# Kernel tuning notes

Measured on AMD Instinct MI355X. Metric: run time of the kernel, lower is better.

## Reference

```python
import jax, jax.numpy as jnp
import numpy as np

K = 3
PAD = 1
STRIDE = 1
DIL = 1


def _bilinear_gather(feat, y, x):
    # feat: [B,C,H,W]; y,x: [B,KK,H,W] sampling coords -> [B,C,KK,H,W]
    B, C, H, W = feat.shape
    feat_flat = feat.reshape(B, C, H * W)
    y0 = jnp.floor(y)
    x0 = jnp.floor(x)
    out = jnp.zeros((B, C) + y.shape[1:], feat.dtype)
    for yi in (y0, y0 + 1.0):
        for xi in (x0, x0 + 1.0):
            wgt = (1.0 - jnp.abs(y - yi)) * (1.0 - jnp.abs(x - xi))
            valid = (yi >= 0) & (yi <= H - 1) & (xi >= 0) & (xi <= W - 1)
            yc = jnp.clip(yi, 0, H - 1).astype(jnp.int32)
            xc = jnp.clip(xi, 0, W - 1).astype(jnp.int32)
            idx = (yc * W + xc).reshape(B, 1, -1)  # [B,1,KK*H*W]
            g = jnp.take_along_axis(feat_flat, idx, axis=2).reshape(B, C, *y.shape[1:])
            out = out + g * (wgt * valid)[:, None]
    return out


def setup_inputs() -> dict:
    key = jax.random.key(0)
    k1, k2, k3, k4, k5 = jax.random.split(key, 5)
    B, Cin, Cout, H, W = 2, 256, 256, 96, 96
    x = jax.random.normal(k1, (B, Cin, H, W), jnp.float32)
    pw_w = jax.random.normal(k2, (Cout, Cin), jnp.float32) / np.sqrt(Cin)
    off_w = jax.random.normal(k3, (2 * K * K, Cout), jnp.float32) * 0.01
    off_b = jax.random.normal(k4, (2 * K * K,), jnp.float32) * 0.5
    dw_w = jax.random.normal(k5, (Cout, K, K), jnp.float32) / K
    return {"x": x, "pw_w": pw_w, "off_w": off_w, "off_b": off_b, "dw_w": dw_w}


def reference(x, pw_w, off_w, off_b, dw_w):
    B, _, H, W = x.shape
    C = pw_w.shape[0]
    # pointwise 1x1 conv (in_channels -> out_channels)
    xp = jnp.einsum("bchw,oc->bohw", x, pw_w)
    # offset 1x1 conv: [B, 2*K*K, H, W], layout (y,x) interleaved per kernel pos
    off = jnp.einsum("bchw,oc->bohw", xp, off_w) + off_b[None, :, None, None]
    off = off.reshape(B, K * K, 2, H, W)
    oy, ox = off[:, :, 0], off[:, :, 1]  # [B,KK,H,W]
    # base sampling grid per kernel position (stride 1, pad 1, dil 1)
    ky, kx = jnp.meshgrid(jnp.arange(K), jnp.arange(K), indexing="ij")
    ky = ky.reshape(-1).astype(jnp.float32)  # [KK]
    kx = kx.reshape(-1).astype(jnp.float32)
    gh = jnp.arange(H, dtype=jnp.float32) * STRIDE - PAD
    gw = jnp.arange(W, dtype=jnp.float32) * STRIDE - PAD
    base_y = gh[None, :, None] + (ky * DIL)[:, None, None]  # [KK,H,1]
    base_x = gw[None, None, :] + (kx * DIL)[:, None, None].transpose(0, 2, 1)  # [KK,1,W]
    y = base_y[None] + oy  # [B,KK,H,W]
    xc = base_x[None] + ox
    sampled = _bilinear_gather(xp, y, xc)  # [B,C,KK,H,W]
    out = jnp.einsum("bckhw,ck->bchw", sampled, dw_w.reshape(C, K * K))
    return out
```

## Files before the change

### kernel.cpp

```cpp
#include <hip/hip_runtime.h>
#include <hip/hip_bf16.h>

#define HWP 9216
#define HH  96
#define WW  96
#define CC  256
#define NB  2

typedef __attribute__((ext_vector_type(8))) short bf16x8;
typedef __attribute__((ext_vector_type(4))) float f32x4;

__device__ inline unsigned short f2bf(float f) {
  union { __hip_bfloat16 h; unsigned short u; } cvt;
  cvt.h = __float2bfloat16(f);
  return cvt.u;
}
__device__ inline float bf_lo(unsigned int u) { return __uint_as_float(u << 16); }
__device__ inline float bf_hi(unsigned int u) { return __uint_as_float(u & 0xffff0000u); }

__global__ __launch_bounds__(256) void k_prep(const float* __restrict__ pw,
                                              const float* __restrict__ ow,
                                              unsigned short* __restrict__ pwb,
                                              unsigned short* __restrict__ wb) {
  int i = (blockIdx.x * 256 + threadIdx.x) * 4;
  if (i < CC * CC) {
    float4 v = *(const float4*)(pw + i);
    ushort4 o = make_ushort4(f2bf(v.x), f2bf(v.y), f2bf(v.z), f2bf(v.w));
    *(ushort4*)(pwb + i) = o;
  } else {
    int j = i - CC * CC;
    int row = j >> 8;
    ushort4 o = make_ushort4(0, 0, 0, 0);
    if (row < 18) {
      float4 v = *(const float4*)(ow + j);
      o = make_ushort4(f2bf(v.x), f2bf(v.y), f2bf(v.z), f2bf(v.w));
    }
    *(ushort4*)(wb + j) = o;
  }
}

__global__ __launch_bounds__(256) void k_main(const float* __restrict__ x,
                                              const unsigned short* __restrict__ pwb,
                                              const unsigned short* __restrict__ wb,
                                              const float* __restrict__ off_b,
                                              unsigned short* __restrict__ xpb,
                                              float* __restrict__ offs) {
  __shared__ unsigned short As[32 * 40];
  __shared__ unsigned short Bs[256 * 40];
  __shared__ unsigned short Cs[32 * 264];

  int b    = blockIdx.z;
  int pix0 = blockIdx.x * 32;
  int t    = threadIdx.x;
  int lane = t & 63;
  int w    = t >> 6;
  int mw = (w & 1) * 16;
  int nw = (w >> 1) * 128;
  int r = lane & 15, q = lane >> 4;

  f32x4 acc[8] = {};

  const float* xg = x + (size_t)b * CC * HWP + pix0;
  int sc = t >> 3;
  int sp = (t & 7) * 4;

  for (int k0 = 0; k0 < CC; k0 += 32) {
    f32x4 xv = __builtin_nontemporal_load((const f32x4*)(xg + (size_t)(k0 + sc) * HWP + sp));
    As[(sp + 0) * 40 + sc] = f2bf(xv.x);
    As[(sp + 1) * 40 + sc] = f2bf(xv.y);
    As[(sp + 2) * 40 + sc] = f2bf(xv.z);
    As[(sp + 3) * 40 + sc] = f2bf(xv.w);
    const unsigned short* bg = pwb + k0;
#pragma unroll
    for (int rep = 0; rep < 4; ++rep) {
      int n  = rep * 64 + (t >> 2);
      int c8 = (t & 3) * 8;
      *(uint4*)&Bs[n * 40 + c8] = *(const uint4*)(bg + n * 256 + c8);
    }
    __syncthreads();
    bf16x8 a = *(const bf16x8*)&As[(mw + r) * 40 + q * 8];
#pragma unroll
    for (int nt = 0; nt < 8; ++nt) {
      bf16x8 bb = *(const bf16x8*)&Bs[(nw + nt * 16 + r) * 40 + q * 8];
      acc[nt] = __builtin_amdgcn_mfma_f32_16x16x32_bf16(a, bb, acc[nt], 0, 0, 0);
    }
    __syncthreads();
  }

#pragma unroll
  for (int nt = 0; nt < 8; ++nt)
#pragma unroll
    for (int rr = 0; rr < 4; ++rr)
      Cs[(mw + q * 4 + rr) * 264 + nw + nt * 16 + r] = f2bf(acc[nt][rr]);
  __syncthreads();

  {
    int pix = t >> 3, c32 = (t & 7) * 32;
    unsigned short* o = xpb + ((size_t)b * HWP + pix0 + pix) * CC + c32;
#pragma unroll
    for (int j = 0; j < 4; ++j)
      *(uint4*)(o + j * 8) = *(const uint4*)&Cs[pix * 264 + c32 + j * 8];
  }

  {
    int mw2 = (w & 1) * 16;
    int nw2 = (w >> 1) * 16;
    f32x4 oacc = {};
#pragma unroll
    for (int ks = 0; ks < CC; ks += 32) {
      bf16x8 a = *(const bf16x8*)&Cs[(mw2 + r) * 264 + ks + q * 8];
      uint4 u = *(const uint4*)(wb + (nw2 + r) * 256 + ks + q * 8);
      bf16x8 bb;
      ((uint4*)&bb)[0] = u;
      oacc = __builtin_amdgcn_mfma_f32_16x16x32_bf16(a, bb, oacc, 0, 0, 0);
    }
    int o = nw2 + r;
    if (o < 18) {
      float ob = off_b[o];
      size_t base = ((size_t)b * HWP + pix0 + mw2 + q * 4) * 20 + o;
#pragma unroll
      for (int rr = 0; rr < 4; ++rr)
        offs[base + (size_t)rr * 20] = oacc[rr] + ob;
    }
  }
}

__global__ __launch_bounds__(256) void k_gather(const unsigned short* __restrict__ xp,
                                                const float* __restrict__ offs,
                                                const float* __restrict__ dw,
                                                float* __restrict__ out) {
  __shared__ float Cs[16][257];
  int bid = blockIdx.x;
  int sb  = (bid & 7) * 144 + (bid >> 3);
  int pix0 = sb * 16;
  int wave = threadIdx.x >> 6;
  int lane = threadIdx.x & 63;
  int c0 = lane * 4;

  float dwr[4][9];
#pragma unroll
  for (int i = 0; i < 4; ++i)
#pragma unroll
    for (int kk = 0; kk < 9; ++kk)
      dwr[i][kk] = dw[(c0 + i) * 9 + kk];

  int b   = pix0 / HWP;
  int hw0 = pix0 - b * HWP;
  const unsigned short* xb = xp + (size_t)b * HWP * CC;

#pragma unroll
  for (int p4 = 0; p4 < 4; ++p4) {
    int ip  = wave * 4 + p4;
    int hw  = hw0 + ip;
    int h   = hw / WW;
    int w   = hw - h * WW;

    const float* op = offs + (size_t)(pix0 + ip) * 20;
    float4 q0 = *(const float4*)(op + 0);
    float4 q1 = *(const float4*)(op + 4);
    float4 q2 = *(const float4*)(op + 8);
    float4 q3 = *(const float4*)(op + 12);
    float2 q4 = *(const float2*)(op + 16);
    float offr[18] = {q0.x,q0.y,q0.z,q0.w, q1.x,q1.y,q1.z,q1.w,
                      q2.x,q2.y,q2.z,q2.w, q3.x,q3.y,q3.z,q3.w, q4.x,q4.y};

    float acc0 = 0.f, acc1 = 0.f, acc2 = 0.f, acc3 = 0.f;
#pragma unroll
    for (int kk = 0; kk < 9; ++kk) {
      float y = (float)(h - 1 + kk / 3) + offr[2 * kk];
      float x = (float)(w - 1 + kk % 3) + offr[2 * kk + 1];
      float y0f = floorf(y), x0f = floorf(x);
      float fy = y - y0f, fx = x - x0f;
      int y0 = (int)y0f, x0 = (int)x0f;
      int y1 = y0 + 1, x1 = x0 + 1;
      bool vy0 = (y0 >= 0) & (y0 < HH);
      bool vy1 = (y1 >= 0) & (y1 < HH);
      bool vx0 = (x0 >= 0) & (x0 < WW);
      bool vx1 = (x1 >= 0) & (x1 < WW);
      int y0c = y0 < 0 ? 0 : (y0 > HH - 1 ? HH - 1 : y0);
      int y1c = y1 < 0 ? 0 : (y1 > HH - 1 ? HH - 1 : y1);
      int x0c = x0 < 0 ? 0 : (x0 > WW - 1 ? WW - 1 : x0);
      int x1c = x1 < 0 ? 0 : (x1 > WW - 1 ? WW - 1 : x1);
      float w00 = (1.f - fy) * (1.f - fx) * ((vy0 && vx0) ? 1.f : 0.f);
      float w01 = (1.f - fy) * fx         * ((vy0 && vx1) ? 1.f : 0.f);
      float w10 = fy * (1.f - fx)         * ((vy1 && vx0) ? 1.f : 0.f);
      float w11 = fy * fx                 * ((vy1 && vx1) ? 1.f : 0.f);

      uint2 u00 = *(const uint2*)(xb + (size_t)(y0c * WW + x0c) * CC + c0);
      uint2 u01 = *(const uint2*)(xb + (size_t)(y0c * WW + x1c) * CC + c0);
      uint2 u10 = *(const uint2*)(xb + (size_t)(y1c * WW + x0c) * CC + c0);
      uint2 u11 = *(const uint2*)(xb + (size_t)(y1c * WW + x1c) * CC + c0);

      float s0 = w00 * bf_lo(u00.x) + w01 * bf_lo(u01.x) + w10 * bf_lo(u10.x) + w11 * bf_lo(u11.x);
      float s1 = w00 * bf_hi(u00.x) + w01 * bf_hi(u01.x) + w10 * bf_hi(u10.x) + w11 * bf_hi(u11.x);
      float s2 = w00 * bf_lo(u00.y) + w01 * bf_lo(u01.y) + w10 * bf_lo(u10.y) + w11 * bf_lo(u11.y);
      float s3 = w00 * bf_hi(u00.y) + w01 * bf_hi(u01.y) + w10 * bf_hi(u10.y) + w11 * bf_hi(u11.y);

      acc0 += dwr[0][kk] * s0;
      acc1 += dwr[1][kk] * s1;
      acc2 += dwr[2][kk] * s2;
      acc3 += dwr[3][kk] * s3;
    }
    *(float4*)&Cs[ip][c0] = make_float4(acc0, acc1, acc2, acc3);
  }
  __syncthreads();
  int ch = threadIdx.x;
  float* ob = out + (size_t)b * CC * HWP + (size_t)ch * HWP + hw0;
#pragma unroll
  for (int p4 = 0; p4 < 4; ++p4) {
    float4 v = make_float4(Cs[p4 * 4 + 0][ch], Cs[p4 * 4 + 1][ch],
                           Cs[p4 * 4 + 2][ch], Cs[p4 * 4 + 3][ch]);
    *(float4*)(ob + p4 * 4) = v;
  }
}

extern "C" void kernel_launch(void* const* d_in, const int* in_sizes, int n_in,
                              void* d_out, int out_size, void* d_ws, size_t ws_size,
                              hipStream_t stream) {
  (void)in_sizes; (void)n_in; (void)out_size; (void)ws_size;
  const float* x     = (const float*)d_in[0];
  const float* pw_w  = (const float*)d_in[1];
  const float* off_w = (const float*)d_in[2];
  const float* off_b = (const float*)d_in[3];
  const float* dw_w  = (const float*)d_in[4];
  float* out = (float*)d_out;

  char* ws = (char*)d_ws;
  unsigned short* xpb = (unsigned short*)ws;
  float* offs = (float*)(ws + 9437184);
  unsigned short* wb  = (unsigned short*)(ws + 10911744);
  unsigned short* pwb = (unsigned short*)(ws + 10928128);

  k_prep <<<(CC * CC + 32 * CC) / 1024, 256, 0, stream>>>(pw_w, off_w, pwb, wb);
  k_main <<<dim3(HWP / 32, 1, NB), 256, 0, stream>>>(x, pwb, wb, off_b, xpb, offs);
  k_gather<<<NB * HWP / 16, 256, 0, stream>>>(xpb, offs, dw_w, out);
}
```

Measured before the change: 131.9 us.

## Prefetch next GEMM k-tile into registers and stage depthwise weights in LDS

In the pointwise GEMM kernel, the global loads for the next 32-wide k slice of x and of the bf16 weights are issued right after the barrier, so they overlap the MFMA work on the current slice. This register double-buffering is meant to hide global memory latency in the main loop. In the gather kernel, the depthwise weights move from 36 per-thread registers into a shared-memory table read as float4, and launch bounds request 4 blocks per CU. This is meant to lower register pressure and raise occupancy, at the cost of extra LDS reads and one more barrier.

```diff
diff --git a/kernel.cpp b/kernel.cpp
--- a/kernel.cpp
+++ b/kernel.cpp
@@ -63,21 +63,30 @@
   const float* xg = x + (size_t)b * CC * HWP + pix0;
   int sc = t >> 3;
   int sp = (t & 7) * 4;
+  int bn = t >> 2;
+  int c8 = (t & 3) * 8;
+
+  f32x4 xv = __builtin_nontemporal_load((const f32x4*)(xg + (size_t)sc * HWP + sp));
+  uint4 bv[4];
+#pragma unroll
+  for (int rep = 0; rep < 4; ++rep)
+    bv[rep] = *(const uint4*)(pwb + (rep * 64 + bn) * 256 + c8);
 
   for (int k0 = 0; k0 < CC; k0 += 32) {
-    f32x4 xv = __builtin_nontemporal_load((const f32x4*)(xg + (size_t)(k0 + sc) * HWP + sp));
     As[(sp + 0) * 40 + sc] = f2bf(xv.x);
     As[(sp + 1) * 40 + sc] = f2bf(xv.y);
     As[(sp + 2) * 40 + sc] = f2bf(xv.z);
     As[(sp + 3) * 40 + sc] = f2bf(xv.w);
-    const unsigned short* bg = pwb + k0;
-#pragma unroll
-    for (int rep = 0; rep < 4; ++rep) {
-      int n  = rep * 64 + (t >> 2);
-      int c8 = (t & 3) * 8;
-      *(uint4*)&Bs[n * 40 + c8] = *(const uint4*)(bg + n * 256 + c8);
-    }
+#pragma unroll
+    for (int rep = 0; rep < 4; ++rep)
+      *(uint4*)&Bs[(rep * 64 + bn) * 40 + c8] = bv[rep];
     __syncthreads();
+    if (k0 + 32 < CC) {
+      xv = __builtin_nontemporal_load((const f32x4*)(xg + (size_t)(k0 + 32 + sc) * HWP + sp));
+#pragma unroll
+      for (int rep = 0; rep < 4; ++rep)
+        bv[rep] = *(const uint4*)(pwb + (rep * 64 + bn) * 256 + k0 + 32 + c8);
+    }
     bf16x8 a = *(const bf16x8*)&As[(mw + r) * 40 + q * 8];
 #pragma unroll
     for (int nt = 0; nt < 8; ++nt) {
@@ -125,11 +134,12 @@
   }
 }
 
-__global__ __launch_bounds__(256) void k_gather(const unsigned short* __restrict__ xp,
-                                                const float* __restrict__ offs,
-                                                const float* __restrict__ dw,
-                                                float* __restrict__ out) {
+__global__ __launch_bounds__(256, 4) void k_gather(const unsigned short* __restrict__ xp,
+                                                   const float* __restrict__ offs,
+                                                   const float* __restrict__ dw,
+                                                   float* __restrict__ out) {
   __shared__ float Cs[16][257];
+  __shared__ float dws[9][256];
   int bid = blockIdx.x;
   int sb  = (bid & 7) * 144 + (bid >> 3);
   int pix0 = sb * 16;
@@ -137,12 +147,13 @@
   int lane = threadIdx.x & 63;
   int c0 = lane * 4;
 
-  float dwr[4][9];
-#pragma unroll
-  for (int i = 0; i < 4; ++i)
+  {
+    int ch = threadIdx.x;
 #pragma unroll
     for (int kk = 0; kk < 9; ++kk)
-      dwr[i][kk] = dw[(c0 + i) * 9 + kk];
+      dws[kk][ch] = dw[ch * 9 + kk];
+  }
+  __syncthreads();
 
   int b   = pix0 / HWP;
   int hw0 = pix0 - b * HWP;
@@ -196,10 +207,11 @@
       float s2 = w00 * bf_lo(u00.y) + w01 * bf_lo(u01.y) + w10 * bf_lo(u10.y) + w11 * bf_lo(u11.y);
       float s3 = w00 * bf_hi(u00.y) + w01 * bf_hi(u01.y) + w10 * bf_hi(u10.y) + w11 * bf_hi(u11.y);
 
-      acc0 += dwr[0][kk] * s0;
-      acc1 += dwr[1][kk] * s1;
-      acc2 += dwr[2][kk] * s2;
-      acc3 += dwr[3][kk] * s3;
+      float4 dv = *(const float4*)&dws[kk][c0];
+      acc0 += dv.x * s0;
+      acc1 += dv.y * s1;
+      acc2 += dv.z * s2;
+      acc3 += dv.w * s3;
     }
     *(float4*)&Cs[ip][c0] = make_float4(acc0, acc1, acc2, acc3);
   }
```

Result: slower. 235.3 us (+78.4%).
